# Kernel tuning notes

Measured on AMD Instinct MI355X. Metric: run time of the kernel, lower is better.

## Reference

```python
import math
import jax, jax.numpy as jnp
import numpy as np

POS_DIM = 32


def _fourier_features(pos, dim):
    # pos: [B, M] in [0,1] -> [B, M, dim]
    half = dim // 2
    freqs = jnp.exp(jnp.linspace(0.0, math.log(1000.0), half, dtype=pos.dtype))
    ang = pos[..., None] * freqs                      # [B, M, half]
    out = jnp.concatenate([jnp.sin(ang), jnp.cos(ang)], axis=-1)
    if out.shape[-1] < dim:  # pad if dim is odd (not the case for dim=32)
        pad = jnp.zeros(out.shape[:-1] + (dim - out.shape[-1],), dtype=pos.dtype)
        out = jnp.concatenate([out, pad], axis=-1)
    return out


def setup_inputs() -> dict:
    key = jax.random.key(0)
    k1, k2, k3 = jax.random.split(key, 3)
    B, T, D, M = 8, 8192, 512, 512
    frame_emb = jax.random.normal(k1, (B, T, D), dtype=jnp.float32)
    beat_bounds = jax.random.randint(k2, (B, M, 2), 0, T).astype(jnp.int64)
    # nn.Linear(D + POS_DIM, D): store as [in, out] for x @ W + b
    bound = 1.0 / math.sqrt(D + POS_DIM)
    W = jax.random.uniform(k3, (D + POS_DIM, D), dtype=jnp.float32,
                           minval=-bound, maxval=bound)
    b = jnp.zeros((D,), dtype=jnp.float32)
    return {"frame_emb": frame_emb, "beat_bounds": beat_bounds, "W": W, "b": b}


def reference(frame_emb, beat_bounds, W, b):
    B, T, D = frame_emb.shape
    M = beat_bounds.shape[1]
    dt = frame_emb.dtype

    # clamp bounds exactly as the torch loop does
    s = jnp.clip(beat_bounds[..., 0], 0, T - 1)                 # [B, M]
    e = jnp.maximum(s + 1, jnp.minimum(beat_bounds[..., 1], T))  # [B, M]

    # segment mean via exclusive cumsum: sum(frame_emb[b, s:e]) = cs[e] - cs[s]
    cs = jnp.concatenate(
        [jnp.zeros((B, 1, D), dtype=dt), jnp.cumsum(frame_emb, axis=1)], axis=1
    )  # [B, T+1, D]
    seg_sum = (jnp.take_along_axis(cs, e[..., None], axis=1)
               - jnp.take_along_axis(cs, s[..., None], axis=1))   # [B, M, D]
    counts = (e - s).astype(dt)[..., None]
    out = seg_sum / counts

    # fourier position features over beat index
    pos = (jnp.arange(M, dtype=dt) / max(1, M - 1)).clip(0.0, 1.0)  # [M]
    ff = _fourier_features(jnp.broadcast_to(pos[None, :], (B, M)), POS_DIM)
    out = jnp.concatenate([out, ff], axis=-1) @ W + b               # [B, M, D]
    return out
```

## Files before the change

### kernel.cpp

```cpp
#include <hip/hip_runtime.h>
#include <math.h>

#define B 8
#define T 8192
#define D 512
#define M 512
#define POS 32
#define CHUNK 4
#define NCHUNK (T / CHUNK)
#define GRP 32
#define NGRP (NCHUNK / GRP)
#define BM (B * M)
#define KD 512

typedef __attribute__((ext_vector_type(8))) short short8;
typedef __attribute__((ext_vector_type(4))) short short4v;
typedef __attribute__((ext_vector_type(4))) float floatx4;

static __device__ inline unsigned short f2bf(float f) {
    unsigned int u = __float_as_uint(f);
    unsigned int r = (u + 0x7fffu + ((u >> 16) & 1u)) >> 16;
    return (unsigned short)r;
}
static __device__ inline float bf2f(unsigned short h) {
    return __uint_as_float(((unsigned int)h) << 16);
}

__global__ __launch_bounds__(256) void k_fusedA(const float* __restrict__ fe,
                                                const float* __restrict__ W,
                                                const float* __restrict__ bias,
                                                float* __restrict__ cp,
                                                float* __restrict__ gsum,
                                                short* __restrict__ WhT,
                                                short* __restrict__ WlT,
                                                float* __restrict__ ffout) {
    int blk = blockIdx.x;
    int tid = threadIdx.x;
    if (blk < 512) {
        int b = blk >> 6;
        int g = blk & 63;
        int d2 = tid << 1;
        const float* src = fe + ((size_t)(b * T + g * (GRP * CHUNK)) * D + d2);
        float* cpb = cp + ((size_t)b * NCHUNK + (size_t)g * GRP) * D + d2;
        float2 acc = {0.f, 0.f};
#pragma unroll 4
        for (int c = 0; c < GRP; ++c) {
#pragma unroll
            for (int r = 0; r < CHUNK; ++r) {
                float2 v = *(const float2*)(src + (size_t)(c * CHUNK + r) * D);
                acc.x += v.x; acc.y += v.y;
            }
            *(float2*)(cpb + (size_t)c * D) = acc;
        }
        *(float2*)(gsum + ((size_t)b * NGRP + g) * D + d2) = acc;
    } else if (blk < 640) {
        __shared__ float ws[32][65];
        int wb = blk - 512;
        int k0 = (wb & 15) * 32;
        int n0 = (wb >> 4) * 64;
        {
            int kk = tid >> 3;
            int nn = (tid & 7) << 3;
            const float* src = W + (size_t)(k0 + kk) * D + n0 + nn;
            float4 v0 = *(const float4*)src;
            float4 v1 = *(const float4*)(src + 4);
            ws[kk][nn + 0] = v0.x; ws[kk][nn + 1] = v0.y; ws[kk][nn + 2] = v0.z; ws[kk][nn + 3] = v0.w;
            ws[kk][nn + 4] = v1.x; ws[kk][nn + 5] = v1.y; ws[kk][nn + 6] = v1.z; ws[kk][nn + 7] = v1.w;
        }
        __syncthreads();
        int n = tid >> 2;
        int kq = (tid & 3) << 3;
        short8 hv, lv;
#pragma unroll
        for (int j = 0; j < 8; ++j) {
            float w = ws[kq + j][n];
            unsigned short hb = f2bf(w);
            hv[j] = (short)hb;
            lv[j] = (short)f2bf(w - bf2f(hb));
        }
        size_t off = (size_t)(n0 + n) * KD + k0 + kq;
        *(short8*)(WhT + off) = hv;
        *(short8*)(WlT + off) = lv;
    } else {
        int m = ((blk - 640) << 1) + (tid >> 7);
        int n4 = (tid & 127) << 2;
        float pos = (float)m * (1.0f / 511.0f);
        float4 acc = *(const float4*)(bias + n4);
#pragma unroll
        for (int j = 0; j < 16; ++j) {
            float freq = expf(0.46051701859880914f * (float)j);
            float ang = pos * freq;
            float s = sinf(ang), c = cosf(ang);
            float4 wsn = *(const float4*)(W + (size_t)(D + j) * D + n4);
            float4 wcn = *(const float4*)(W + (size_t)(D + 16 + j) * D + n4);
            acc.x += s * wsn.x + c * wcn.x;
            acc.y += s * wsn.y + c * wcn.y;
            acc.z += s * wsn.z + c * wcn.z;
            acc.w += s * wsn.w + c * wcn.w;
        }
        *(float4*)(ffout + (size_t)m * D + n4) = acc;
    }
}

__global__ __launch_bounds__(64) void k_scan_coarse(const float* __restrict__ gsum,
                                                    float* __restrict__ gx) {
    int b = blockIdx.x >> 3;
    int d = ((blockIdx.x & 7) << 6) + threadIdx.x;
    const float* gs = gsum + (size_t)b * NGRP * D + d;
    float* gxp = gx + (size_t)b * (NGRP + 1) * D + d;
    float acc = 0.f;
#pragma unroll
    for (int g = 0; g < NGRP; ++g) {
        gxp[(size_t)g * D] = acc;
        acc += gs[(size_t)g * D];
    }
    gxp[(size_t)NGRP * D] = acc;
}

__global__ __launch_bounds__(128) void k_buildx(const float* __restrict__ fe,
                                                const int* __restrict__ bounds,
                                                const float* __restrict__ cp,
                                                const float* __restrict__ gx,
                                                short* __restrict__ Xh,
                                                short* __restrict__ Xl) {
    int bm = blockIdx.x;
    int b = bm / M;
    int b0 = bounds[bm * 2 + 0];
    int b1 = bounds[bm * 2 + 1];
    int s = min(max(b0, 0), T - 1);
    int e = max(min(b1, T), s + 1);
    int cs_ = s >> 2, ce = e >> 2;
    int d4 = threadIdx.x << 2;

    const float* cpb = cp + (size_t)b * NCHUNK * D;
    const float* gxb = gx + (size_t)b * (NGRP + 1) * D;

    float4 acc = *(const float4*)(gxb + (size_t)(ce >> 5) * D + d4);
    if (ce & 31) {
        float4 v = *(const float4*)(cpb + (size_t)(ce - 1) * D + d4);
        acc.x += v.x; acc.y += v.y; acc.z += v.z; acc.w += v.w;
    }
    {
        float4 p = *(const float4*)(gxb + (size_t)(cs_ >> 5) * D + d4);
        acc.x -= p.x; acc.y -= p.y; acc.z -= p.z; acc.w -= p.w;
        if (cs_ & 31) {
            float4 v = *(const float4*)(cpb + (size_t)(cs_ - 1) * D + d4);
            acc.x -= v.x; acc.y -= v.y; acc.z -= v.z; acc.w -= v.w;
        }
    }

    const float* feb = fe + (size_t)b * T * D + d4;
    for (int t = ce * CHUNK; t < e; ++t) {
        float4 v = *(const float4*)(feb + (size_t)t * D);
        acc.x += v.x; acc.y += v.y; acc.z += v.z; acc.w += v.w;
    }
    for (int t = cs_ * CHUNK; t < s; ++t) {
        float4 v = *(const float4*)(feb + (size_t)t * D);
        acc.x -= v.x; acc.y -= v.y; acc.z -= v.z; acc.w -= v.w;
    }
    float inv = 1.0f / (float)(e - s);
    float x0 = acc.x * inv, x1 = acc.y * inv, x2 = acc.z * inv, x3 = acc.w * inv;

    unsigned short h0 = f2bf(x0), h1 = f2bf(x1), h2 = f2bf(x2), h3 = f2bf(x3);
    short4v hv, lv;
    hv[0] = (short)h0; hv[1] = (short)h1; hv[2] = (short)h2; hv[3] = (short)h3;
    lv[0] = (short)f2bf(x0 - bf2f(h0));
    lv[1] = (short)f2bf(x1 - bf2f(h1));
    lv[2] = (short)f2bf(x2 - bf2f(h2));
    lv[3] = (short)f2bf(x3 - bf2f(h3));
    size_t off = (size_t)bm * KD + d4;
    *(short4v*)(Xh + off) = hv;
    *(short4v*)(Xl + off) = lv;
}

#define BK 64
__global__ __launch_bounds__(256) void k_gemm(const short* __restrict__ Xh,
                                              const short* __restrict__ Xl,
                                              const short* __restrict__ WhT,
                                              const short* __restrict__ WlT,
                                              const float* __restrict__ ffout,
                                              float* __restrict__ out) {
    __shared__ short Ah[2][64 * 32], Al[2][64 * 32];
    __shared__ short Bh[2][64 * 32], Bl[2][64 * 32];
    int n0 = (blockIdx.x & 7) << 6;
    int m0 = (blockIdx.x >> 3) << 6;
    int tid = threadIdx.x;
    int w = tid >> 6;
    int l = tid & 63;
    int lm = l & 15;
    int q = l >> 4;
    int wm = (w & 1) << 5;
    int wn = (w >> 1) << 5;

    floatx4 acc[2][2];
#pragma unroll
    for (int i = 0; i < 2; ++i)
#pragma unroll
        for (int j = 0; j < 2; ++j)
            acc[i][j] = (floatx4){0.f, 0.f, 0.f, 0.f};

    int srow = tid >> 2;
    int skq = tid & 3;
    int sslot = skq ^ ((srow >> 1) & 3);
    int ldsoff = (srow << 5) + (sslot << 3);
    const short* gXh = Xh + (size_t)(m0 + srow) * KD + (skq << 3);
    const short* gXl = Xl + (size_t)(m0 + srow) * KD + (skq << 3);
    const short* gBh = WhT + (size_t)(n0 + srow) * KD + (skq << 3);
    const short* gBl = WlT + (size_t)(n0 + srow) * KD + (skq << 3);

    int aoff[2], boff[2];
#pragma unroll
    for (int mt = 0; mt < 2; ++mt) {
        int row = wm + (mt << 4) + lm;
        aoff[mt] = (row << 5) + ((q ^ ((row >> 1) & 3)) << 3);
    }
#pragma unroll
    for (int nt = 0; nt < 2; ++nt) {
        int row = wn + (nt << 4) + lm;
        boff[nt] = (row << 5) + ((q ^ ((row >> 1) & 3)) << 3);
    }

    short8 pxh[2], pxl[2], pbh[2], pbl[2];
#pragma unroll
    for (int h = 0; h < 2; ++h) {
        pxh[h] = *(const short8*)(gXh + (h << 5));
        pxl[h] = *(const short8*)(gXl + (h << 5));
        pbh[h] = *(const short8*)(gBh + (h << 5));
        pbl[h] = *(const short8*)(gBl + (h << 5));
    }

    for (int k0 = 0; k0 < KD; k0 += BK) {
        __syncthreads();
#pragma unroll
        for (int h = 0; h < 2; ++h) {
            *(short8*)(&Ah[h][ldsoff]) = pxh[h];
            *(short8*)(&Al[h][ldsoff]) = pxl[h];
            *(short8*)(&Bh[h][ldsoff]) = pbh[h];
            *(short8*)(&Bl[h][ldsoff]) = pbl[h];
        }
        __syncthreads();

        int kn = k0 + BK;
        if (kn < KD) {
#pragma unroll
            for (int h = 0; h < 2; ++h) {
                pxh[h] = *(const short8*)(gXh + kn + (h << 5));
                pxl[h] = *(const short8*)(gXl + kn + (h << 5));
                pbh[h] = *(const short8*)(gBh + kn + (h << 5));
                pbl[h] = *(const short8*)(gBl + kn + (h << 5));
            }
        }

#pragma unroll
        for (int h = 0; h < 2; ++h) {
            short8 ah[2], al[2], bh[2], bl[2];
#pragma unroll
            for (int mt = 0; mt < 2; ++mt) {
                ah[mt] = *(const short8*)(&Ah[h][aoff[mt]]);
                al[mt] = *(const short8*)(&Al[h][aoff[mt]]);
            }
#pragma unroll
            for (int nt = 0; nt < 2; ++nt) {
                bh[nt] = *(const short8*)(&Bh[h][boff[nt]]);
                bl[nt] = *(const short8*)(&Bl[h][boff[nt]]);
            }
#pragma unroll
            for (int mt = 0; mt < 2; ++mt)
#pragma unroll
                for (int nt = 0; nt < 2; ++nt) {
                    acc[mt][nt] = __builtin_amdgcn_mfma_f32_16x16x32_bf16(
                        ah[mt], bh[nt], acc[mt][nt], 0, 0, 0);
                    acc[mt][nt] = __builtin_amdgcn_mfma_f32_16x16x32_bf16(
                        ah[mt], bl[nt], acc[mt][nt], 0, 0, 0);
                    acc[mt][nt] = __builtin_amdgcn_mfma_f32_16x16x32_bf16(
                        al[mt], bh[nt], acc[mt][nt], 0, 0, 0);
                }
        }
    }

#pragma unroll
    for (int mt = 0; mt < 2; ++mt) {
#pragma unroll
        for (int nt = 0; nt < 2; ++nt) {
            int gcol = n0 + wn + (nt << 4) + lm;
#pragma unroll
            for (int r = 0; r < 4; ++r) {
                int grow = m0 + wm + (mt << 4) + (q << 2) + r;
                float f = ffout[(size_t)(grow & (M - 1)) * D + gcol];
                out[(size_t)grow * D + gcol] = acc[mt][nt][r] + f;
            }
        }
    }
}

extern "C" void kernel_launch(void* const* d_in, const int* in_sizes, int n_in,
                              void* d_out, int out_size, void* d_ws, size_t ws_size,
                              hipStream_t stream) {
    const float* fe = (const float*)d_in[0];
    const int* bounds = (const int*)d_in[1];
    const float* W = (const float*)d_in[2];
    const float* bias = (const float*)d_in[3];
    float* out = (float*)d_out;

    float* cp = (float*)d_ws;
    float* gsum = cp + (size_t)B * NCHUNK * D;
    float* gx = gsum + (size_t)B * NGRP * D;
    float* ffout = gx + (size_t)B * (NGRP + 1) * D;
    short* Xh = (short*)(ffout + (size_t)M * D);
    short* Xl = Xh + (size_t)BM * KD;
    short* WhT = Xl + (size_t)BM * KD;
    short* WlT = WhT + (size_t)KD * D;

    k_fusedA<<<896, 256, 0, stream>>>(fe, W, bias, cp, gsum, WhT, WlT, ffout);
    k_scan_coarse<<<B * 8, 64, 0, stream>>>(gsum, gx);
    k_buildx<<<BM, 128, 0, stream>>>(fe, bounds, cp, gx, Xh, Xl);
    k_gemm<<<64 * 8, 256, 0, stream>>>(Xh, Xl, WhT, WlT, ffout, out);
}
```

Before: 227.3 us.

## Fuse four kernels into one cooperative persistent kernel with grid syncs

Replaces the four launches (chunk prefix sums and weight split, coarse scan, segment-mean build, split-bf16 GEMM) with a single cooperative kernel of 256 blocks that loops over each phase's jobs and separates phases with grid.sync. The goal is to remove launch gaps and inter-kernel drain between small phases. In exchange, each phase now runs on only 256 blocks at one block per CU, so the build and GEMM stages have less parallelism and fewer waves to hide latency. If the cooperative launch fails, it falls back to the original four launches.

```diff
diff --git a/kernel.cpp b/kernel.cpp
--- a/kernel.cpp
+++ b/kernel.cpp
@@ -1,5 +1,8 @@
 #include <hip/hip_runtime.h>
+#include <hip/hip_cooperative_groups.h>
 #include <math.h>
+
+namespace cg = cooperative_groups;
 
 #define B 8
 #define T 8192
@@ -12,6 +15,7 @@
 #define NGRP (NCHUNK / GRP)
 #define BM (B * M)
 #define KD 512
+#define BK 64
 
 typedef __attribute__((ext_vector_type(8))) short short8;
 typedef __attribute__((ext_vector_type(4))) short short4v;
@@ -24,6 +28,288 @@
 }
 static __device__ inline float bf2f(unsigned short h) {
     return __uint_as_float(((unsigned int)h) << 16);
+}
+
+__global__ __launch_bounds__(256, 1) void k_mega(
+        const float* __restrict__ fe, const int* __restrict__ bounds,
+        const float* __restrict__ W, const float* __restrict__ bias,
+        float* __restrict__ cp, float* __restrict__ gsum,
+        float* __restrict__ gx, float* __restrict__ ffout,
+        short* __restrict__ Xh, short* __restrict__ Xl,
+        short* __restrict__ WhT, short* __restrict__ WlT,
+        float* __restrict__ out) {
+    cg::grid_group grid = cg::this_grid();
+    __shared__ short smem[16384];
+    int blk = blockIdx.x;
+    int tid = threadIdx.x;
+
+#pragma unroll 1
+    for (int job = blk; job < 896; job += 256) {
+        if (job < 512) {
+            int b = job >> 6;
+            int g = job & 63;
+            int d2 = tid << 1;
+            const float* src = fe + ((size_t)(b * T + g * (GRP * CHUNK)) * D + d2);
+            float* cpb = cp + ((size_t)b * NCHUNK + (size_t)g * GRP) * D + d2;
+            float2 acc = {0.f, 0.f};
+#pragma unroll 4
+            for (int c = 0; c < GRP; ++c) {
+#pragma unroll
+                for (int r = 0; r < CHUNK; ++r) {
+                    float2 v = *(const float2*)(src + (size_t)(c * CHUNK + r) * D);
+                    acc.x += v.x; acc.y += v.y;
+                }
+                *(float2*)(cpb + (size_t)c * D) = acc;
+            }
+            *(float2*)(gsum + ((size_t)b * NGRP + g) * D + d2) = acc;
+        } else if (job < 640) {
+            float* ws = (float*)smem;
+            int wb = job - 512;
+            int k0 = (wb & 15) * 32;
+            int n0 = (wb >> 4) * 64;
+            __syncthreads();
+            {
+                int kk = tid >> 3;
+                int nn = (tid & 7) << 3;
+                const float* src = W + (size_t)(k0 + kk) * D + n0 + nn;
+                float4 v0 = *(const float4*)src;
+                float4 v1 = *(const float4*)(src + 4);
+                float* wr = ws + kk * 65 + nn;
+                wr[0] = v0.x; wr[1] = v0.y; wr[2] = v0.z; wr[3] = v0.w;
+                wr[4] = v1.x; wr[5] = v1.y; wr[6] = v1.z; wr[7] = v1.w;
+            }
+            __syncthreads();
+            int n = tid >> 2;
+            int kq = (tid & 3) << 3;
+            short8 hv, lv;
+#pragma unroll
+            for (int j = 0; j < 8; ++j) {
+                float wv = ws[(kq + j) * 65 + n];
+                unsigned short hb = f2bf(wv);
+                hv[j] = (short)hb;
+                lv[j] = (short)f2bf(wv - bf2f(hb));
+            }
+            size_t off = (size_t)(n0 + n) * KD + k0 + kq;
+            *(short8*)(WhT + off) = hv;
+            *(short8*)(WlT + off) = lv;
+        } else {
+            int m = ((job - 640) << 1) + (tid >> 7);
+            int n4 = (tid & 127) << 2;
+            float pos = (float)m * (1.0f / 511.0f);
+            float4 acc = *(const float4*)(bias + n4);
+#pragma unroll
+            for (int j = 0; j < 16; ++j) {
+                float freq = expf(0.46051701859880914f * (float)j);
+                float ang = pos * freq;
+                float s = sinf(ang), c = cosf(ang);
+                float4 wsn = *(const float4*)(W + (size_t)(D + j) * D + n4);
+                float4 wcn = *(const float4*)(W + (size_t)(D + 16 + j) * D + n4);
+                acc.x += s * wsn.x + c * wcn.x;
+                acc.y += s * wsn.y + c * wcn.y;
+                acc.z += s * wsn.z + c * wcn.z;
+                acc.w += s * wsn.w + c * wcn.w;
+            }
+            *(float4*)(ffout + (size_t)m * D + n4) = acc;
+        }
+    }
+    __threadfence();
+    grid.sync();
+
+    {
+        int gt = blk * 256 + tid;
+        if (gt < B * D) {
+            int b = gt >> 9;
+            int d = gt & 511;
+            const float* gs = gsum + (size_t)b * NGRP * D + d;
+            float* gxp = gx + (size_t)b * (NGRP + 1) * D + d;
+            float acc = 0.f;
+#pragma unroll
+            for (int g = 0; g < NGRP; ++g) {
+                gxp[(size_t)g * D] = acc;
+                acc += gs[(size_t)g * D];
+            }
+            gxp[(size_t)NGRP * D] = acc;
+        }
+    }
+    __threadfence();
+    grid.sync();
+
+    {
+        int sub = (blk << 1) + (tid >> 7);
+        int d4 = (tid & 127) << 2;
+#pragma unroll 1
+        for (int i = 0; i < 8; ++i) {
+            int bm = sub + (i << 9);
+            int b = bm >> 9;
+            int b0 = bounds[bm * 2 + 0];
+            int b1 = bounds[bm * 2 + 1];
+            int s = min(max(b0, 0), T - 1);
+            int e = max(min(b1, T), s + 1);
+            int cs_ = s >> 2, ce = e >> 2;
+
+            const float* cpb = cp + (size_t)b * NCHUNK * D;
+            const float* gxb = gx + (size_t)b * (NGRP + 1) * D;
+
+            float4 acc = *(const float4*)(gxb + (size_t)(ce >> 5) * D + d4);
+            if (ce & 31) {
+                float4 v = *(const float4*)(cpb + (size_t)(ce - 1) * D + d4);
+                acc.x += v.x; acc.y += v.y; acc.z += v.z; acc.w += v.w;
+            }
+            {
+                float4 p = *(const float4*)(gxb + (size_t)(cs_ >> 5) * D + d4);
+                acc.x -= p.x; acc.y -= p.y; acc.z -= p.z; acc.w -= p.w;
+                if (cs_ & 31) {
+                    float4 v = *(const float4*)(cpb + (size_t)(cs_ - 1) * D + d4);
+                    acc.x -= v.x; acc.y -= v.y; acc.z -= v.z; acc.w -= v.w;
+                }
+            }
+
+            const float* feb = fe + (size_t)b * T * D + d4;
+            for (int t = ce * CHUNK; t < e; ++t) {
+                float4 v = *(const float4*)(feb + (size_t)t * D);
+                acc.x += v.x; acc.y += v.y; acc.z += v.z; acc.w += v.w;
+            }
+            for (int t = cs_ * CHUNK; t < s; ++t) {
+                float4 v = *(const float4*)(feb + (size_t)t * D);
+                acc.x -= v.x; acc.y -= v.y; acc.z -= v.z; acc.w -= v.w;
+            }
+            float inv = 1.0f / (float)(e - s);
+            float x0 = acc.x * inv, x1 = acc.y * inv, x2 = acc.z * inv, x3 = acc.w * inv;
+
+            unsigned short h0 = f2bf(x0), h1 = f2bf(x1), h2 = f2bf(x2), h3 = f2bf(x3);
+            short4v hv, lv;
+            hv[0] = (short)h0; hv[1] = (short)h1; hv[2] = (short)h2; hv[3] = (short)h3;
+            lv[0] = (short)f2bf(x0 - bf2f(h0));
+            lv[1] = (short)f2bf(x1 - bf2f(h1));
+            lv[2] = (short)f2bf(x2 - bf2f(h2));
+            lv[3] = (short)f2bf(x3 - bf2f(h3));
+            size_t off = (size_t)bm * KD + d4;
+            *(short4v*)(Xh + off) = hv;
+            *(short4v*)(Xl + off) = lv;
+        }
+    }
+    __threadfence();
+    grid.sync();
+
+#define AH(h) (smem + (h) * 8192)
+#define ALr(h) (smem + (h) * 8192 + 2048)
+#define BH(h) (smem + (h) * 8192 + 4096)
+#define BLr(h) (smem + (h) * 8192 + 6144)
+    {
+        int w = tid >> 6;
+        int l = tid & 63;
+        int lm = l & 15;
+        int q = l >> 4;
+        int wm = (w & 1) << 5;
+        int wn = (w >> 1) << 5;
+        int srow = tid >> 2;
+        int skq = tid & 3;
+        int sslot = skq ^ ((srow >> 1) & 3);
+        int ldsoff = (srow << 5) + (sslot << 3);
+
+        int aoff[2], boff[2];
+#pragma unroll
+        for (int mt = 0; mt < 2; ++mt) {
+            int row = wm + (mt << 4) + lm;
+            aoff[mt] = (row << 5) + ((q ^ ((row >> 1) & 3)) << 3);
+        }
+#pragma unroll
+        for (int nt = 0; nt < 2; ++nt) {
+            int row = wn + (nt << 4) + lm;
+            boff[nt] = (row << 5) + ((q ^ ((row >> 1) & 3)) << 3);
+        }
+
+#pragma unroll 1
+        for (int rep = 0; rep < 2; ++rep) {
+            int tile = blk + (rep << 8);
+            int n0 = (tile & 7) << 6;
+            int m0 = (tile >> 3) << 6;
+
+            floatx4 acc[2][2];
+#pragma unroll
+            for (int i = 0; i < 2; ++i)
+#pragma unroll
+                for (int j = 0; j < 2; ++j)
+                    acc[i][j] = (floatx4){0.f, 0.f, 0.f, 0.f};
+
+            const short* gXh = Xh + (size_t)(m0 + srow) * KD + (skq << 3);
+            const short* gXl = Xl + (size_t)(m0 + srow) * KD + (skq << 3);
+            const short* gBh = WhT + (size_t)(n0 + srow) * KD + (skq << 3);
+            const short* gBl = WlT + (size_t)(n0 + srow) * KD + (skq << 3);
+
+            short8 pxh[2], pxl[2], pbh[2], pbl[2];
+#pragma unroll
+            for (int h = 0; h < 2; ++h) {
+                pxh[h] = *(const short8*)(gXh + (h << 5));
+                pxl[h] = *(const short8*)(gXl + (h << 5));
+                pbh[h] = *(const short8*)(gBh + (h << 5));
+                pbl[h] = *(const short8*)(gBl + (h << 5));
+            }
+
+            for (int k0 = 0; k0 < KD; k0 += BK) {
+                __syncthreads();
+#pragma unroll
+                for (int h = 0; h < 2; ++h) {
+                    *(short8*)(AH(h) + ldsoff) = pxh[h];
+                    *(short8*)(ALr(h) + ldsoff) = pxl[h];
+                    *(short8*)(BH(h) + ldsoff) = pbh[h];
+                    *(short8*)(BLr(h) + ldsoff) = pbl[h];
+                }
+                __syncthreads();
+
+                int kn = k0 + BK;
+                if (kn < KD) {
+#pragma unroll
+                    for (int h = 0; h < 2; ++h) {
+                        pxh[h] = *(const short8*)(gXh + kn + (h << 5));
+                        pxl[h] = *(const short8*)(gXl + kn + (h << 5));
+                        pbh[h] = *(const short8*)(gBh + kn + (h << 5));
+                        pbl[h] = *(const short8*)(gBl + kn + (h << 5));
+                    }
+                }
+
+#pragma unroll
+                for (int h = 0; h < 2; ++h) {
+                    short8 ah[2], al[2], bh[2], bl[2];
+#pragma unroll
+                    for (int mt = 0; mt < 2; ++mt) {
+                        ah[mt] = *(const short8*)(AH(h) + aoff[mt]);
+                        al[mt] = *(const short8*)(ALr(h) + aoff[mt]);
+                    }
+#pragma unroll
+                    for (int nt = 0; nt < 2; ++nt) {
+                        bh[nt] = *(const short8*)(BH(h) + boff[nt]);
+                        bl[nt] = *(const short8*)(BLr(h) + boff[nt]);
+                    }
+#pragma unroll
+                    for (int mt = 0; mt < 2; ++mt)
+#pragma unroll
+                        for (int nt = 0; nt < 2; ++nt) {
+                            acc[mt][nt] = __builtin_amdgcn_mfma_f32_16x16x32_bf16(
+                                ah[mt], bh[nt], acc[mt][nt], 0, 0, 0);
+                            acc[mt][nt] = __builtin_amdgcn_mfma_f32_16x16x32_bf16(
+                                ah[mt], bl[nt], acc[mt][nt], 0, 0, 0);
+                            acc[mt][nt] = __builtin_amdgcn_mfma_f32_16x16x32_bf16(
+                                al[mt], bh[nt], acc[mt][nt], 0, 0, 0);
+                        }
+                }
+            }
+
+#pragma unroll
+            for (int mt = 0; mt < 2; ++mt) {
+#pragma unroll
+                for (int nt = 0; nt < 2; ++nt) {
+                    int gcol = n0 + wn + (nt << 4) + lm;
+#pragma unroll
+                    for (int r = 0; r < 4; ++r) {
+                        int grow = m0 + wm + (mt << 4) + (q << 2) + r;
+                        float f = ffout[(size_t)(grow & (M - 1)) * D + gcol];
+                        out[(size_t)grow * D + gcol] = acc[mt][nt][r] + f;
+                    }
+                }
+            }
+        }
+    }
 }
 
 __global__ __launch_bounds__(256) void k_fusedA(const float* __restrict__ fe,
@@ -173,7 +459,6 @@
     *(short4v*)(Xl + off) = lv;
 }
 
-#define BK 64
 __global__ __launch_bounds__(256) void k_gemm(const short* __restrict__ Xh,
                                               const short* __restrict__ Xl,
                                               const short* __restrict__ WhT,
@@ -311,8 +596,17 @@
     short* WhT = Xl + (size_t)BM * KD;
     short* WlT = WhT + (size_t)KD * D;
 
-    k_fusedA<<<896, 256, 0, stream>>>(fe, W, bias, cp, gsum, WhT, WlT, ffout);
-    k_scan_coarse<<<B * 8, 64, 0, stream>>>(gsum, gx);
-    k_buildx<<<BM, 128, 0, stream>>>(fe, bounds, cp, gx, Xh, Xl);
-    k_gemm<<<64 * 8, 256, 0, stream>>>(Xh, Xl, WhT, WlT, ffout, out);
-}
+    void* args[] = {(void*)&fe, (void*)&bounds, (void*)&W, (void*)&bias,
+                    (void*)&cp, (void*)&gsum, (void*)&gx, (void*)&ffout,
+                    (void*)&Xh, (void*)&Xl, (void*)&WhT, (void*)&WlT,
+                    (void*)&out};
+    hipError_t rc = hipLaunchCooperativeKernel((void*)k_mega, dim3(256),
+                                               dim3(256), args, 0, stream);
+    if (rc != hipSuccess) {
+        (void)hipGetLastError();
+        k_fusedA<<<896, 256, 0, stream>>>(fe, W, bias, cp, gsum, WhT, WlT, ffout);
+        k_scan_coarse<<<B * 8, 64, 0, stream>>>(gsum, gx);
+        k_buildx<<<BM, 128, 0, stream>>>(fe, bounds, cp, gx, Xh, Xl);
+        k_gemm<<<64 * 8, 256, 0, stream>>>(Xh, Xl, WhT, WlT, ffout, out);
+    }
+}
```

After: 494.4 us. 2.18x slower.
